# Kernel tuning notes

Measured on AMD Instinct MI355X. Metric: run time of the kernel, lower is better.

The kernel has to match this reference:

```python
import jax, jax.numpy as jnp
import numpy as np

B = 4; E_PER = 100_000; E = B * E_PER
N_NODES = 50_000; N_REL = 500; D = 64; D_LG = 256
K_PER_VI = 20; S_VI = E // K_PER_VI          # 20000 sorted vi segments
S_VJ_PER = 5_000; S_VJ = B * S_VJ_PER        # 20000 unsorted vj segments
N_MEM = 131_072
INTERACT = ((0, 3), (0, 2, 3), (0, 4), (0, 2, 4), (1, 3), (1, 2, 3), (1, 4), (1, 2, 4))


def _build_edges():
    rng = np.random.default_rng(0)
    idx_vi = np.repeat(np.arange(S_VI), K_PER_VI)          # sorted segment ids
    gpb = S_VI // B
    eg = idx_vi // gpb                                     # sorted by eg_idx too
    vi = rng.integers(0, N_NODES, S_VI)[idx_vi]
    idx_vj = np.empty(E, dtype=np.int64)
    for b in range(B):
        loc = np.concatenate([np.arange(S_VJ_PER), rng.integers(0, S_VJ_PER, E_PER - S_VJ_PER)])
        rng.shuffle(loc)
        idx_vj[b * E_PER:(b + 1) * E_PER] = b * S_VJ_PER + loc  # every group non-empty
    vj = rng.integers(0, N_NODES, S_VJ)[idx_vj]            # consistent (eg, vj) per group
    rel = rng.integers(0, N_REL, E)
    e2vi = rng.integers(0, N_MEM, E)
    e2vj = rng.integers(0, N_MEM, E)
    return np.stack([eg, vi, vj, rel, idx_vi, idx_vj, e2vi, e2vj], axis=1).astype(np.int32)


def setup_inputs() -> dict:
    key = jax.random.key(0)
    ks = jax.random.split(key, 10)
    return {
        "node_attention": jax.random.uniform(ks[0], (B, N_NODES), jnp.float32),
        "scanned_edges": jnp.asarray(_build_edges()),
        "edges_y": jax.random.uniform(ks[1], (E,), jnp.float32),
        "hidden_uncon": jax.random.normal(ks[2], (1, N_NODES, D_LG), jnp.float32),
        "hidden_con": jax.random.normal(ks[3], (N_MEM, D), jnp.float32),
        "Wc": jax.random.normal(ks[4], (D, D), jnp.float32) / np.sqrt(D).astype(np.float32),
        "bc": jnp.zeros((D,), jnp.float32),
        "Wu": jax.random.normal(ks[5], (D_LG, D), jnp.float32) / np.sqrt(D_LG).astype(np.float32),
        "bu": jnp.zeros((D,), jnp.float32),
        "rel_table": jax.random.normal(ks[6], (N_REL, D), jnp.float32) * 0.05,
        "ws": jax.random.normal(ks[7], (len(INTERACT), D), jnp.float32) / np.sqrt(float(len(INTERACT))).astype(np.float32) if False else jax.random.normal(ks[7], (len(INTERACT), D), jnp.float32) * (1.0 / np.sqrt(len(INTERACT)).astype(np.float32)),
        "fb": jnp.zeros((D,), jnp.float32),
        "out_w": jax.random.normal(ks[8], (D,), jnp.float32),
        "out_b": jnp.zeros((D,), jnp.float32),
        "n_vi_segments": S_VI,
        "n_vj_segments": S_VJ,
    }


def reference(node_attention, scanned_edges, edges_y, hidden_uncon, hidden_con,
              Wc, bc, Wu, bu, rel_table, ws, fb, out_w, out_b,
              n_vi_segments, n_vj_segments):
    eg, vi, vj, rel = (scanned_edges[:, i] for i in range(4))
    idx_vi, idx_vj, e2vi, e2vj = (scanned_edges[:, i] for i in range(4, 8))
    # projections (proj_con / proj_uncon, tanh Dense)
    hc = jnp.tanh(hidden_con @ Wc + bc)          # [N_MEM, D]
    hu = jnp.tanh(hidden_uncon @ Wu + bu)[0]     # [n_nodes, D]; batch_size==1 path of Node2Edge
    # Node2Edge gathers
    feats = (hc[e2vi], hu[vi], rel_table[rel], hc[e2vj], hu[vj])  # each [E, D]
    # F layer: weighted sum of elementwise interaction products
    out = fb
    for k, idxs in enumerate(INTERACT):
        x = feats[idxs[0]]
        for i in idxs[1:]:
            x = x * feats[i]
        out = out + x * ws[k]
    out = jax.nn.relu(out) * out_w + out_b
    logits = jnp.sum(out, axis=1)                # [E]
    # NeighborSoftmax at 'vi' (sorted segment softmax)
    m = jax.ops.segment_max(logits, idx_vi, num_segments=n_vi_segments)
    ex = jnp.exp(logits - m[idx_vi])
    den = jax.ops.segment_sum(ex, idx_vi, num_segments=n_vi_segments)
    transition = ex / den[idx_vi]
    # attention flow: gather source attention, weight, aggregate at vj
    trans_att = transition * node_attention[eg, vi] * edges_y
    aggr = jax.ops.segment_sum(trans_att, idx_vj, num_segments=n_vj_segments)
    b_g = jax.ops.segment_max(eg, idx_vj, num_segments=n_vj_segments)
    vj_g = jax.ops.segment_max(vj, idx_vj, num_segments=n_vj_segments)
    new_node_attention = jnp.zeros_like(node_attention).at[b_g, vj_g].add(aggr)
    return new_node_attention
```

## Files before the change

kernel.cpp:

```cpp
#include <hip/hip_runtime.h>
#include <hip/hip_bf16.h>
#include <hip/hip_fp16.h>

#define D 64
#define KPER 20

typedef __attribute__((ext_vector_type(8))) short short8;
typedef __attribute__((ext_vector_type(4))) float floatx4;

__device__ __forceinline__ unsigned short f2bfu(float x) {
    __hip_bfloat16 h = __float2bfloat16(x);
    return *reinterpret_cast<unsigned short*>(&h);
}
__device__ __forceinline__ unsigned short f2hu(float x) {
    __half h = __float2half(x);
    return *reinterpret_cast<unsigned short*>(&h);
}
union UH2 { unsigned u; __half2 h; };
__device__ __forceinline__ __half2 u2h2(unsigned u) { UH2 x; x.u = u; return x.h; }
__device__ __forceinline__ unsigned pick4(uint4 v, int p) {
    return p == 0 ? v.x : p == 1 ? v.y : p == 2 ? v.z : v.w;
}

__device__ __forceinline__ unsigned cvt2bf(float lo, float hi) {
    unsigned r;
    asm("v_cvt_pk_bf16_f32 %0, %1, %2" : "=v"(r) : "v"(lo), "v"(hi));
    return r;
}

__device__ __forceinline__ __half2 pk_max(__half2 a, __half2 b) {
    __half2 r;
    asm("v_pk_max_f16 %0, %1, %2" : "=v"(r) : "v"(a), "v"(b));
    return r;
}

__device__ __forceinline__ float fast_tanh(float x) {
    float xc = fminf(fmaxf(x, -15.f), 15.f);
    float e = __expf(2.f * xc);
    return 1.f - 2.f * __builtin_amdgcn_rcpf(1.f + e);
}

template<int CTRL>
__device__ __forceinline__ float dpp_add(float x) {
    int t = __builtin_amdgcn_update_dpp(0, __float_as_int(x), CTRL, 0xf, 0xf, true);
    return x + __int_as_float(t);
}
template<int CTRL>
__device__ __forceinline__ float dpp_max(float x) {
    int xi = __float_as_int(x);
    int t = __builtin_amdgcn_update_dpp(xi, xi, CTRL, 0xf, 0xf, false);
    return fmaxf(x, __int_as_float(t));
}
__device__ __forceinline__ float wave_sum_b(float x) {
    x = dpp_add<0x111>(x); x = dpp_add<0x112>(x);
    x = dpp_add<0x114>(x); x = dpp_add<0x118>(x);
    x = dpp_add<0x142>(x); x = dpp_add<0x143>(x);
    return __int_as_float(__builtin_amdgcn_readlane(__float_as_int(x), 63));
}
__device__ __forceinline__ float wave_max_b(float x) {
    x = dpp_max<0x111>(x); x = dpp_max<0x112>(x);
    x = dpp_max<0x114>(x); x = dpp_max<0x118>(x);
    x = dpp_max<0x142>(x); x = dpp_max<0x143>(x);
    return __int_as_float(__builtin_amdgcn_readlane(__float_as_int(x), 63));
}
__device__ __forceinline__ float row8_sum(float x) {
    x = dpp_add<0x111>(x); x = dpp_add<0x112>(x);
    x = dpp_add<0x114>(x);
    return x;
}

__global__ __launch_bounds__(256) void prep(
        const float* __restrict__ Wc, const float* __restrict__ Wu,
        const float* __restrict__ relf, const float* __restrict__ wsf,
        const float* __restrict__ fbf,
        unsigned short* __restrict__ Wcp, unsigned short* __restrict__ Wup,
        unsigned short* __restrict__ relb, unsigned short* __restrict__ wsh,
        unsigned short* __restrict__ fbh, float* __restrict__ outz,
        int nout, int nrel) {
    int tid = blockIdx.x * 256 + threadIdx.x;
    int nth = gridDim.x * 256;
    for (int i = tid; i < 4 * 2 * 64 * 8; i += nth) {
        int j = i & 7, lane = (i >> 3) & 63, f = i >> 9;
        int ct = f >> 1, kt = f & 1;
        int m = lane & 15, quad = lane >> 4;
        Wcp[i] = f2bfu(Wc[(kt * 32 + quad * 8 + j) * 64 + ct * 16 + m]);
    }
    for (int i = tid; i < 4 * 8 * 64 * 8; i += nth) {
        int j = i & 7, lane = (i >> 3) & 63, f = i >> 9;
        int ct = f >> 3, kt = f & 7;
        int m = lane & 15, quad = lane >> 4;
        Wup[i] = f2bfu(Wu[(kt * 32 + quad * 8 + j) * 64 + ct * 16 + m]);
    }
    for (int i = tid; i < nrel; i += nth) relb[i] = f2hu(relf[i]);
    for (int i = tid; i < 8 * D; i += nth) wsh[i] = f2hu(wsf[i]);
    for (int i = tid; i < D; i += nth) fbh[i] = f2hu(fbf[i]);
    for (int i = tid; i < nout; i += nth) outz[i] = 0.0f;
}

__device__ __forceinline__ void proj64_pair(const float* __restrict__ h,
        const unsigned short* __restrict__ Wp, const float* __restrict__ b,
        unsigned short* __restrict__ out, int rt0) {
    constexpr int K = 64, KT = 2, CTN = 4;
    int lane = threadIdx.x & 63;
    int m = lane & 15, quad = lane >> 4;
    short8 bfr[CTN][KT];
    #pragma unroll
    for (int ct = 0; ct < CTN; ++ct)
        #pragma unroll
        for (int kt = 0; kt < KT; ++kt)
            bfr[ct][kt] = *(const short8*)(Wp + (((ct * 2 + kt) * 64 + lane) << 3));
    float bv[CTN];
    #pragma unroll
    for (int ct = 0; ct < CTN; ++ct) bv[ct] = b[ct * 16 + m];
    int rt1 = rt0 + 1;
    const float* hrow0 = h + (size_t)(rt0 * 16 + m) * K + quad * 8;
    const float* hrow1 = h + (size_t)(rt1 * 16 + m) * K + quad * 8;
    floatx4 a0[KT][2], a1[KT][2];
    #pragma unroll
    for (int kt = 0; kt < KT; ++kt) {
        a0[kt][0] = *(const floatx4*)(hrow0 + kt * 32);
        a0[kt][1] = *(const floatx4*)(hrow0 + kt * 32 + 4);
        a1[kt][0] = *(const floatx4*)(hrow1 + kt * 32);
        a1[kt][1] = *(const floatx4*)(hrow1 + kt * 32 + 4);
    }
    #pragma unroll
    for (int t = 0; t < 2; ++t) {
        floatx4 (*ar)[2] = t ? a1 : a0;
        int rt = t ? rt1 : rt0;
        floatx4 acc[CTN];
        #pragma unroll
        for (int ct = 0; ct < CTN; ++ct) acc[ct] = floatx4{0.f, 0.f, 0.f, 0.f};
        #pragma unroll
        for (int kt = 0; kt < KT; ++kt) {
            union { uint4 u; short8 s; } cc;
            cc.u.x = cvt2bf(ar[kt][0][0], ar[kt][0][1]);
            cc.u.y = cvt2bf(ar[kt][0][2], ar[kt][0][3]);
            cc.u.z = cvt2bf(ar[kt][1][0], ar[kt][1][1]);
            cc.u.w = cvt2bf(ar[kt][1][2], ar[kt][1][3]);
            short8 af = cc.s;
            #pragma unroll
            for (int ct = 0; ct < CTN; ++ct)
                acc[ct] = __builtin_amdgcn_mfma_f32_16x16x32_bf16(af, bfr[ct][kt], acc[ct], 0, 0, 0);
        }
        #pragma unroll
        for (int ct = 0; ct < CTN; ++ct) {
            int col = ct * 16 + m;
            #pragma unroll
            for (int reg = 0; reg < 4; ++reg) {
                int row = rt * 16 + quad * 4 + reg;
                out[(size_t)row * 64 + col] = f2hu(fast_tanh(acc[ct][reg] + bv[ct]));
            }
        }
    }
}

__device__ __forceinline__ void proj256_one(const float* __restrict__ h,
        const unsigned short* Wlds, const float* __restrict__ b,
        unsigned short* __restrict__ out, int ct0, int rt) {
    constexpr int K = 256, KT = 8, CTN = 2;
    int lane = threadIdx.x & 63;
    int m = lane & 15, quad = lane >> 4;
    float bv[CTN];
    #pragma unroll
    for (int ct = 0; ct < CTN; ++ct) bv[ct] = b[(ct0 + ct) * 16 + m];
    floatx4 acc[CTN];
    #pragma unroll
    for (int ct = 0; ct < CTN; ++ct) acc[ct] = floatx4{0.f, 0.f, 0.f, 0.f};
    const float* hrow = h + (size_t)(rt * 16 + m) * K + quad * 8;
    #pragma unroll
    for (int kt = 0; kt < KT; ++kt) {
        floatx4 v0 = *(const floatx4*)(hrow + kt * 32);
        floatx4 v1 = *(const floatx4*)(hrow + kt * 32 + 4);
        short8 b0 = *(const short8*)(Wlds + ((((ct0 + 0) * 8 + kt) * 64 + lane) << 3));
        short8 b1 = *(const short8*)(Wlds + ((((ct0 + 1) * 8 + kt) * 64 + lane) << 3));
        union { uint4 u; short8 s; } cc;
        cc.u.x = cvt2bf(v0[0], v0[1]);
        cc.u.y = cvt2bf(v0[2], v0[3]);
        cc.u.z = cvt2bf(v1[0], v1[1]);
        cc.u.w = cvt2bf(v1[2], v1[3]);
        short8 af = cc.s;
        acc[0] = __builtin_amdgcn_mfma_f32_16x16x32_bf16(af, b0, acc[0], 0, 0, 0);
        acc[1] = __builtin_amdgcn_mfma_f32_16x16x32_bf16(af, b1, acc[1], 0, 0, 0);
    }
    #pragma unroll
    for (int ct = 0; ct < CTN; ++ct) {
        int col = (ct0 + ct) * 16 + m;
        #pragma unroll
        for (int reg = 0; reg < 4; ++reg) {
            int row = rt * 16 + quad * 4 + reg;
            out[(size_t)row * 64 + col] = f2hu(fast_tanh(acc[ct][reg] + bv[ct]));
        }
    }
}

__global__ __launch_bounds__(256) void proj_fused(
        const float* __restrict__ hcon, const unsigned short* __restrict__ Wcp,
        const float* __restrict__ bc,
        const float* __restrict__ hun, const unsigned short* __restrict__ Wup,
        const float* __restrict__ bu,
        unsigned short* __restrict__ hc, unsigned short* __restrict__ hu,
        int t256, int g256b) {
    __shared__ __align__(16) unsigned short Wlds[16384];
    int bid = blockIdx.x;
    int w = threadIdx.x >> 6;
    if (bid < g256b) {
        const uint4* src = (const uint4*)Wup;
        uint4* dst = (uint4*)Wlds;
        #pragma unroll
        for (int i = 0; i < 8; ++i)
            dst[threadIdx.x + i * 256] = src[threadIdx.x + i * 256];
        __syncthreads();
        int task = bid * 4 + w;
        if (task < 2 * t256)
            proj256_one(hun, Wlds, bu, hu, (task & 1) * 2, task >> 1);
    } else {
        int wid = (bid - g256b) * 4 + w;
        proj64_pair(hcon, Wcp, bc, hc, wid * 2);
    }
}

__device__ __forceinline__ float edge_acc8(
        uint4 G0, uint4 G2, uint4 G3, uint4 G4, uint4 F1,
        const uint4* __restrict__ wk4, uint4 fb4,
        floatx4 ow0, floatx4 ow1, __half2 z2) {
    float acc = 0.f;
    #pragma unroll
    for (int p = 0; p < 4; ++p) {
        __half2 F0 = u2h2(pick4(G0, p));
        __half2 F2 = u2h2(pick4(G2, p));
        __half2 F3 = u2h2(pick4(G3, p));
        __half2 F4 = u2h2(pick4(G4, p));
        __half2 f1 = u2h2(pick4(F1, p));
        __half2 fb2 = u2h2(pick4(fb4, p));
        __half2 w0 = u2h2(pick4(wk4[0], p));
        __half2 w1 = u2h2(pick4(wk4[1], p));
        __half2 w2 = u2h2(pick4(wk4[2], p));
        __half2 w3 = u2h2(pick4(wk4[3], p));
        __half2 w4 = u2h2(pick4(wk4[4], p));
        __half2 w5 = u2h2(pick4(wk4[5], p));
        __half2 w6 = u2h2(pick4(wk4[6], p));
        __half2 w7 = u2h2(pick4(wk4[7], p));
        __half2 t1 = __hfma2(F2, w1, w0);
        __half2 t2 = __hfma2(F2, w5, w4);
        __half2 t3 = __hfma2(F2, w3, w2);
        __half2 t4 = __hfma2(F2, w7, w6);
        __half2 uu = __hfma2(F0, t1, __hmul2(f1, t2));
        __half2 vv = __hfma2(F0, t3, __hmul2(f1, t4));
        __half2 od = __hfma2(F3, uu, __hfma2(F4, vv, fb2));
        __half2 r  = pk_max(od, z2);
        float2 rf  = __half22float2(r);
        float owa = (p < 2) ? ow0[2 * p]     : ow1[2 * p - 4];
        float owb = (p < 2) ? ow0[2 * p + 1] : ow1[2 * p - 3];
        acc = fmaf(rf.x, owa, fmaf(rf.y, owb, acc));
    }
    return acc;
}

__global__ __launch_bounds__(256, 3) void edge_kernel(
        const float* __restrict__ natt, const int* __restrict__ edges,
        const float* __restrict__ ey, const unsigned short* __restrict__ hc,
        const unsigned short* __restrict__ hu, const unsigned short* __restrict__ relt,
        const unsigned short* __restrict__ wsh, const unsigned short* __restrict__ fbh,
        const float* __restrict__ outw, float* __restrict__ out, int N) {
    int lane = threadIdx.x & 63;
    int g8 = lane >> 3, sub8 = lane & 7;
    int wid = blockIdx.x * 4 + (threadIdx.x >> 6);
    long baseA = (long)(wid * 2) * KPER;
    long baseB = baseA + KPER;
    const int* ebA = edges + baseA * 8;
    const int* ebB = edges + baseB * 8;

    int2 h0A = *(const int2*)ebA;
    int2 h0B = *(const int2*)ebB;
    int2 m23A[3], m67A[3], m23B[3], m67B[3];
    #pragma unroll
    for (int t = 0; t < 3; ++t) {
        int e = t * 8 + g8; e = (e < KPER) ? e : (KPER - 1);
        m23A[t] = *(const int2*)(ebA + e * 8 + 2);
        m67A[t] = *(const int2*)(ebA + e * 8 + 6);
        m23B[t] = *(const int2*)(ebB + e * 8 + 2);
        m67B[t] = *(const int2*)(ebB + e * 8 + 6);
    }
    int myvjA = 0, myvjB = 0; float eyA = 0.f, eyB = 0.f;
    if (lane < KPER) {
        myvjA = ebA[lane * 8 + 2];
        myvjB = ebB[lane * 8 + 2];
        eyA = ey[baseA + lane];
        eyB = ey[baseB + lane];
    }
    int egA = __builtin_amdgcn_readfirstlane(h0A.x);
    int viA = __builtin_amdgcn_readfirstlane(h0A.y);
    int egB = __builtin_amdgcn_readfirstlane(h0B.x);
    int viB = __builtin_amdgcn_readfirstlane(h0B.y);

    uint4 GA0[3], GA2[3], GA3[3], GA4[3];
    #pragma unroll
    for (int t = 0; t < 3; ++t) {
        GA0[t] = *(const uint4*)(hc   + (size_t)m67A[t].x * D + sub8 * 8);
        GA2[t] = *(const uint4*)(relt + (size_t)m23A[t].y * D + sub8 * 8);
        GA3[t] = *(const uint4*)(hc   + (size_t)m67A[t].y * D + sub8 * 8);
        GA4[t] = *(const uint4*)(hu   + (size_t)m23A[t].x * D + sub8 * 8);
    }
    uint4 F1A = *(const uint4*)(hu + (size_t)viA * D + sub8 * 8);
    uint4 GB0[3], GB2[3], GB3[3], GB4[3];
    #pragma unroll
    for (int t = 0; t < 3; ++t) {
        GB0[t] = *(const uint4*)(hc   + (size_t)m67B[t].x * D + sub8 * 8);
        GB2[t] = *(const uint4*)(relt + (size_t)m23B[t].y * D + sub8 * 8);
        GB3[t] = *(const uint4*)(hc   + (size_t)m67B[t].y * D + sub8 * 8);
        GB4[t] = *(const uint4*)(hu   + (size_t)m23B[t].x * D + sub8 * 8);
    }
    uint4 F1B = *(const uint4*)(hu + (size_t)viB * D + sub8 * 8);
    float naA = natt[(size_t)egA * N + viA];
    float naB = natt[(size_t)egB * N + viB];

    uint4 wk4[8];
    #pragma unroll
    for (int k = 0; k < 8; ++k) wk4[k] = *(const uint4*)(wsh + k * D + sub8 * 8);
    uint4 fb4 = *(const uint4*)(fbh + sub8 * 8);
    floatx4 ow0 = *(const floatx4*)(outw + sub8 * 8);
    floatx4 ow1 = *(const floatx4*)(outw + sub8 * 8 + 4);
    __half2 z2 = __float2half2_rn(0.f);

    float mylA = -INFINITY, mylB = -INFINITY;
    #pragma unroll
    for (int t = 0; t < 3; ++t) {
        float acc = edge_acc8(GA0[t], GA2[t], GA3[t], GA4[t], F1A, wk4, fb4, ow0, ow1, z2);
        float rs = row8_sum(acc);
        float tot = __shfl(rs, ((lane & 7) << 3) + 7);
        mylA = ((lane >> 3) == t && lane < KPER) ? tot : mylA;
    }
    float mxA = wave_max_b(mylA);
    float exA = __expf(mylA - mxA);
    float denA = wave_sum_b(exA);
    if (lane < KPER) {
        float tv = (exA / denA) * naA * eyA;
        atomicAdd(out + (size_t)egA * N + myvjA, tv);
    }
    #pragma unroll
    for (int t = 0; t < 3; ++t) {
        float acc = edge_acc8(GB0[t], GB2[t], GB3[t], GB4[t], F1B, wk4, fb4, ow0, ow1, z2);
        float rs = row8_sum(acc);
        float tot = __shfl(rs, ((lane & 7) << 3) + 7);
        mylB = ((lane >> 3) == t && lane < KPER) ? tot : mylB;
    }
    float mxB = wave_max_b(mylB);
    float exB = __expf(mylB - mxB);
    float denB = wave_sum_b(exB);
    if (lane < KPER) {
        float tv = (exB / denB) * naB * eyB;
        atomicAdd(out + (size_t)egB * N + myvjB, tv);
    }
}

extern "C" void kernel_launch(void* const* d_in, const int* in_sizes, int n_in,
                              void* d_out, int out_size, void* d_ws, size_t ws_size,
                              hipStream_t stream) {
    const float* natt = (const float*)d_in[0];
    const int*   edges = (const int*)d_in[1];
    const float* ey   = (const float*)d_in[2];
    const float* hun  = (const float*)d_in[3];
    const float* hcon = (const float*)d_in[4];
    const float* Wc   = (const float*)d_in[5];
    const float* bc   = (const float*)d_in[6];
    const float* Wu   = (const float*)d_in[7];
    const float* bu   = (const float*)d_in[8];
    const float* relt = (const float*)d_in[9];
    const float* wsm  = (const float*)d_in[10];
    const float* fb   = (const float*)d_in[11];
    const float* outw = (const float*)d_in[12];
    float* out = (float*)d_out;

    int E    = in_sizes[2];
    int S    = E / KPER;
    int nmem = in_sizes[4] / D;
    int N    = in_sizes[3] / 256;
    int nrel = in_sizes[9];

    int t64  = nmem / 16;
    int t256 = N / 16;
    int g64  = t64 / 8;
    int g256b = (2 * t256 + 3) / 4;

    unsigned short* hc  = (unsigned short*)d_ws;
    unsigned short* hu  = hc + (size_t)nmem * D;
    unsigned short* rb  = hu + (size_t)N * D;
    unsigned short* Wcp = rb + nrel;
    unsigned short* Wup = Wcp + 4096;
    unsigned short* wsh = Wup + 16384;
    unsigned short* fbh = wsh + 8 * D;

    prep<<<64, 256, 0, stream>>>(Wc, Wu, relt, wsm, fb, Wcp, Wup, rb, wsh, fbh,
                                 out, out_size, nrel);
    proj_fused<<<g256b + g64, 256, 0, stream>>>(hcon, Wcp, bc, hun, Wup, bu,
                                                hc, hu, t256, g256b);
    edge_kernel<<<S / 8, 256, 0, stream>>>(natt, edges, ey, hc, hu, rb,
                                           wsh, fbh, outw, out, N);
}
```

Before: 190.1 us.

## Split 256-wide projection into quarter tasks and stage Wc in LDS

The fused projection kernel now launches 512-thread blocks. Each wave of the 256-input projection computes one 16-column quarter of a row tile instead of half, which creates more independent tasks and lowers per-wave register pressure. The 64-input projection now stages its packed weights in shared memory and processes one row tile per wave instead of two. In exchange, each hidden_uncon row tile is read by four waves instead of two, and every block pays a shared-memory fill and barrier.

```diff
diff --git a/kernel.cpp b/kernel.cpp
--- a/kernel.cpp
+++ b/kernel.cpp
@@ -97,72 +97,15 @@
     for (int i = tid; i < nout; i += nth) outz[i] = 0.0f;
 }
 
-__device__ __forceinline__ void proj64_pair(const float* __restrict__ h,
-        const unsigned short* __restrict__ Wp, const float* __restrict__ b,
-        unsigned short* __restrict__ out, int rt0) {
+__device__ __forceinline__ void proj64_one(const float* __restrict__ h,
+        const unsigned short* Wlds, const float* __restrict__ b,
+        unsigned short* __restrict__ out, int rt) {
     constexpr int K = 64, KT = 2, CTN = 4;
     int lane = threadIdx.x & 63;
     int m = lane & 15, quad = lane >> 4;
-    short8 bfr[CTN][KT];
-    #pragma unroll
-    for (int ct = 0; ct < CTN; ++ct)
-        #pragma unroll
-        for (int kt = 0; kt < KT; ++kt)
-            bfr[ct][kt] = *(const short8*)(Wp + (((ct * 2 + kt) * 64 + lane) << 3));
     float bv[CTN];
     #pragma unroll
     for (int ct = 0; ct < CTN; ++ct) bv[ct] = b[ct * 16 + m];
-    int rt1 = rt0 + 1;
-    const float* hrow0 = h + (size_t)(rt0 * 16 + m) * K + quad * 8;
-    const float* hrow1 = h + (size_t)(rt1 * 16 + m) * K + quad * 8;
-    floatx4 a0[KT][2], a1[KT][2];
-    #pragma unroll
-    for (int kt = 0; kt < KT; ++kt) {
-        a0[kt][0] = *(const floatx4*)(hrow0 + kt * 32);
-        a0[kt][1] = *(const floatx4*)(hrow0 + kt * 32 + 4);
-        a1[kt][0] = *(const floatx4*)(hrow1 + kt * 32);
-        a1[kt][1] = *(const floatx4*)(hrow1 + kt * 32 + 4);
-    }
-    #pragma unroll
-    for (int t = 0; t < 2; ++t) {
-        floatx4 (*ar)[2] = t ? a1 : a0;
-        int rt = t ? rt1 : rt0;
-        floatx4 acc[CTN];
-        #pragma unroll
-        for (int ct = 0; ct < CTN; ++ct) acc[ct] = floatx4{0.f, 0.f, 0.f, 0.f};
-        #pragma unroll
-        for (int kt = 0; kt < KT; ++kt) {
-            union { uint4 u; short8 s; } cc;
-            cc.u.x = cvt2bf(ar[kt][0][0], ar[kt][0][1]);
-            cc.u.y = cvt2bf(ar[kt][0][2], ar[kt][0][3]);
-            cc.u.z = cvt2bf(ar[kt][1][0], ar[kt][1][1]);
-            cc.u.w = cvt2bf(ar[kt][1][2], ar[kt][1][3]);
-            short8 af = cc.s;
-            #pragma unroll
-            for (int ct = 0; ct < CTN; ++ct)
-                acc[ct] = __builtin_amdgcn_mfma_f32_16x16x32_bf16(af, bfr[ct][kt], acc[ct], 0, 0, 0);
-        }
-        #pragma unroll
-        for (int ct = 0; ct < CTN; ++ct) {
-            int col = ct * 16 + m;
-            #pragma unroll
-            for (int reg = 0; reg < 4; ++reg) {
-                int row = rt * 16 + quad * 4 + reg;
-                out[(size_t)row * 64 + col] = f2hu(fast_tanh(acc[ct][reg] + bv[ct]));
-            }
-        }
-    }
-}
-
-__device__ __forceinline__ void proj256_one(const float* __restrict__ h,
-        const unsigned short* Wlds, const float* __restrict__ b,
-        unsigned short* __restrict__ out, int ct0, int rt) {
-    constexpr int K = 256, KT = 8, CTN = 2;
-    int lane = threadIdx.x & 63;
-    int m = lane & 15, quad = lane >> 4;
-    float bv[CTN];
-    #pragma unroll
-    for (int ct = 0; ct < CTN; ++ct) bv[ct] = b[(ct0 + ct) * 16 + m];
     floatx4 acc[CTN];
     #pragma unroll
     for (int ct = 0; ct < CTN; ++ct) acc[ct] = floatx4{0.f, 0.f, 0.f, 0.f};
@@ -171,20 +114,21 @@
     for (int kt = 0; kt < KT; ++kt) {
         floatx4 v0 = *(const floatx4*)(hrow + kt * 32);
         floatx4 v1 = *(const floatx4*)(hrow + kt * 32 + 4);
-        short8 b0 = *(const short8*)(Wlds + ((((ct0 + 0) * 8 + kt) * 64 + lane) << 3));
-        short8 b1 = *(const short8*)(Wlds + ((((ct0 + 1) * 8 + kt) * 64 + lane) << 3));
         union { uint4 u; short8 s; } cc;
         cc.u.x = cvt2bf(v0[0], v0[1]);
         cc.u.y = cvt2bf(v0[2], v0[3]);
         cc.u.z = cvt2bf(v1[0], v1[1]);
         cc.u.w = cvt2bf(v1[2], v1[3]);
         short8 af = cc.s;
-        acc[0] = __builtin_amdgcn_mfma_f32_16x16x32_bf16(af, b0, acc[0], 0, 0, 0);
-        acc[1] = __builtin_amdgcn_mfma_f32_16x16x32_bf16(af, b1, acc[1], 0, 0, 0);
+        #pragma unroll
+        for (int ct = 0; ct < CTN; ++ct) {
+            short8 bfr = *(const short8*)(Wlds + (((ct * 2 + kt) * 64 + lane) << 3));
+            acc[ct] = __builtin_amdgcn_mfma_f32_16x16x32_bf16(af, bfr, acc[ct], 0, 0, 0);
+        }
     }
     #pragma unroll
     for (int ct = 0; ct < CTN; ++ct) {
-        int col = (ct0 + ct) * 16 + m;
+        int col = ct * 16 + m;
         #pragma unroll
         for (int reg = 0; reg < 4; ++reg) {
             int row = rt * 16 + quad * 4 + reg;
@@ -193,29 +137,61 @@
     }
 }
 
-__global__ __launch_bounds__(256) void proj_fused(
+__device__ __forceinline__ void proj256_quarter(const float* __restrict__ h,
+        const unsigned short* Wlds, const float* __restrict__ b,
+        unsigned short* __restrict__ out, int ct, int rt) {
+    constexpr int K = 256, KT = 8;
+    int lane = threadIdx.x & 63;
+    int m = lane & 15, quad = lane >> 4;
+    float bv = b[ct * 16 + m];
+    floatx4 acc = floatx4{0.f, 0.f, 0.f, 0.f};
+    const float* hrow = h + (size_t)(rt * 16 + m) * K + quad * 8;
+    #pragma unroll
+    for (int kt = 0; kt < KT; ++kt) {
+        floatx4 v0 = *(const floatx4*)(hrow + kt * 32);
+        floatx4 v1 = *(const floatx4*)(hrow + kt * 32 + 4);
+        short8 bfr = *(const short8*)(Wlds + (((ct * 8 + kt) * 64 + lane) << 3));
+        union { uint4 u; short8 s; } cc;
+        cc.u.x = cvt2bf(v0[0], v0[1]);
+        cc.u.y = cvt2bf(v0[2], v0[3]);
+        cc.u.z = cvt2bf(v1[0], v1[1]);
+        cc.u.w = cvt2bf(v1[2], v1[3]);
+        acc = __builtin_amdgcn_mfma_f32_16x16x32_bf16(cc.s, bfr, acc, 0, 0, 0);
+    }
+    int col = ct * 16 + m;
+    #pragma unroll
+    for (int reg = 0; reg < 4; ++reg) {
+        int row = rt * 16 + quad * 4 + reg;
+        out[(size_t)row * 64 + col] = f2hu(fast_tanh(acc[reg] + bv));
+    }
+}
+
+__global__ __launch_bounds__(512, 8) void proj_fused(
         const float* __restrict__ hcon, const unsigned short* __restrict__ Wcp,
         const float* __restrict__ bc,
         const float* __restrict__ hun, const unsigned short* __restrict__ Wup,
         const float* __restrict__ bu,
         unsigned short* __restrict__ hc, unsigned short* __restrict__ hu,
-        int t256, int g256b) {
-    __shared__ __align__(16) unsigned short Wlds[16384];
+        int t256, int g256q) {
+    __shared__ __align__(16) uint4 WldsU[2048];
     int bid = blockIdx.x;
     int w = threadIdx.x >> 6;
-    if (bid < g256b) {
+    if (bid < g256q) {
         const uint4* src = (const uint4*)Wup;
-        uint4* dst = (uint4*)Wlds;
         #pragma unroll
-        for (int i = 0; i < 8; ++i)
-            dst[threadIdx.x + i * 256] = src[threadIdx.x + i * 256];
+        for (int i = 0; i < 4; ++i)
+            WldsU[threadIdx.x + i * 512] = src[threadIdx.x + i * 512];
         __syncthreads();
-        int task = bid * 4 + w;
-        if (task < 2 * t256)
-            proj256_one(hun, Wlds, bu, hu, (task & 1) * 2, task >> 1);
+        int task = bid * 8 + w;
+        if (task < 4 * t256)
+            proj256_quarter(hun, (const unsigned short*)WldsU, bu, hu,
+                            task & 3, task >> 2);
     } else {
-        int wid = (bid - g256b) * 4 + w;
-        proj64_pair(hcon, Wcp, bc, hc, wid * 2);
+        const uint4* src = (const uint4*)Wcp;
+        WldsU[threadIdx.x] = src[threadIdx.x];
+        __syncthreads();
+        int rt = (bid - g256q) * 8 + w;
+        proj64_one(hcon, (const unsigned short*)WldsU, bc, hc, rt);
     }
 }
 
@@ -380,7 +356,7 @@
     int t64  = nmem / 16;
     int t256 = N / 16;
     int g64  = t64 / 8;
-    int g256b = (2 * t256 + 3) / 4;
+    int g256q = (4 * t256 + 7) / 8;
 
     unsigned short* hc  = (unsigned short*)d_ws;
     unsigned short* hu  = hc + (size_t)nmem * D;
@@ -392,8 +368,8 @@
 
     prep<<<64, 256, 0, stream>>>(Wc, Wu, relt, wsm, fb, Wcp, Wup, rb, wsh, fbh,
                                  out, out_size, nrel);
-    proj_fused<<<g256b + g64, 256, 0, stream>>>(hcon, Wcp, bc, hun, Wup, bu,
-                                                hc, hu, t256, g256b);
+    proj_fused<<<g256q + g64, 512, 0, stream>>>(hcon, Wcp, bc, hun, Wup, bu,
+                                                hc, hu, t256, g256q);
     edge_kernel<<<S / 8, 256, 0, stream>>>(natt, edges, ey, hc, hu, rb,
                                            wsh, fbh, outw, out, N);
 }
```

Result: slower. 204.8 us (+7.7%).
